# Kernel tuning notes

Hardware: AMD Instinct MI355X
Metric: run time of the kernel (lower is better)

Reference implementation:

```python
import jax, jax.numpy as jnp
import numpy as np

B, S, D = 1, 2048, 4096
H, KV, HD = 32, 8, 128
C = 4096  # cache length
THETA = 1000000.0
NEG = -1e9


def setup_inputs() -> dict:
    key = jax.random.key(0)
    ks = jax.random.split(key, 8)
    std = 0.02
    x = jax.random.normal(ks[0], (B, S, D), jnp.float32)
    wq = jax.random.normal(ks[1], (H * HD, D), jnp.float32) * std
    wk = jax.random.normal(ks[2], (KV * HD, D), jnp.float32) * std
    wv = jax.random.normal(ks[3], (KV * HD, D), jnp.float32) * std
    wo = jax.random.normal(ks[4], (D, H * HD), jnp.float32) * std
    k_cache = jnp.zeros((B, KV, C, HD), jnp.float32)
    v_cache = jnp.zeros((B, KV, C, HD), jnp.float32)
    # rotary tables (real/imag of freqs_cis)
    inv_freq = 1.0 / (THETA ** (jnp.arange(0, HD, 2, dtype=jnp.float32) / HD))  # [HD/2]
    t = jnp.arange(C, dtype=jnp.float32)
    freqs = jnp.outer(t, inv_freq)  # [C, HD/2]
    cos, sin = jnp.cos(freqs), jnp.sin(freqs)
    # causal additive mask over cache positions
    mask = jnp.where(jnp.tril(jnp.ones((C, C), bool)), 0.0, NEG).astype(jnp.float32)
    storage_idx = jnp.arange(S, dtype=jnp.int32)
    return {"x": x, "wq": wq, "wk": wk, "wv": wv, "wo": wo,
            "k_cache": k_cache, "v_cache": v_cache,
            "cos": cos, "sin": sin, "mask": mask, "storage_idx": storage_idx}


def _rope(x, cos, sin):
    # x: [B, h, S, HD]; cos/sin: [S, HD/2] -> complex mult on interleaved pairs
    xr, xi = x[..., 0::2], x[..., 1::2]
    c = cos[None, None, :, :]
    s = sin[None, None, :, :]
    or_, oi_ = xr * c - xi * s, xr * s + xi * c
    return jnp.stack([or_, oi_], axis=-1).reshape(x.shape)


def reference(x, wq, wk, wv, wo, k_cache, v_cache, cos, sin, mask, storage_idx):
    bsz, seqlen, _ = x.shape
    xq = jnp.einsum('bsd,ed->bse', x, wq).reshape(bsz, seqlen, H, HD).transpose(0, 2, 1, 3)
    xk = jnp.einsum('bsd,ed->bse', x, wk).reshape(bsz, seqlen, KV, HD).transpose(0, 2, 1, 3)
    xv = jnp.einsum('bsd,ed->bse', x, wv).reshape(bsz, seqlen, KV, HD).transpose(0, 2, 1, 3)
    cos_g, sin_g = cos[storage_idx], sin[storage_idx]
    xq = _rope(xq, cos_g, sin_g)
    xk = _rope(xk, cos_g, sin_g)
    # scatter into KV cache at storage_idx along the position axis
    keys = k_cache.at[:, :, storage_idx, :].set(xk)
    values = v_cache.at[:, :, storage_idx, :].set(xv)
    # GQA: repeat kv heads (kv-head-major, matches expand+reshape)
    rep = H // KV
    keys = jnp.repeat(keys, rep, axis=1)      # [B, H, C, HD]
    values = jnp.repeat(values, rep, axis=1)  # [B, H, C, HD]
    scores = jnp.einsum('bhqd,bhkd->bhqk', xq, keys) / np.sqrt(HD)
    scores = scores + mask[storage_idx][None, None, :, :]
    attn = jax.nn.softmax(scores, axis=-1)
    out = jnp.einsum('bhqk,bhkd->bhqd', attn, values)
    out = out.transpose(0, 2, 1, 3).reshape(bsz, seqlen, H * HD)
    return jnp.einsum('bse,de->bsd', out, wo)
```

## Files before the change

kernel.cpp:

```cpp
#include <hip/hip_runtime.h>
#include <cstdint>
#include <cstddef>

#define S_LEN 2048
#define DM    4096
#define NH    32
#define NKV   8
#define HDIM  128
#define EQ    4096
#define EKV   1024
#define SCALE 0.08838834764831845f
#define SC_LOG2E 0.1275325477889277f

typedef unsigned short u16;
typedef short bf16x8 __attribute__((ext_vector_type(8)));
typedef float f32x4  __attribute__((ext_vector_type(4)));

__device__ __forceinline__ u16 f2bf(float f) {
  union { float f; unsigned u; } v; v.f = f;
  unsigned r = v.u + 0x7FFFu + ((v.u >> 16) & 1u);
  return (u16)(r >> 16);
}
__device__ __forceinline__ float bf2f(u16 b) {
  union { unsigned u; float f; } v; v.u = ((unsigned)b) << 16;
  return v.f;
}
__device__ __forceinline__ void glds16(const void* g, void* l) {
  __builtin_amdgcn_global_load_lds((const __attribute__((address_space(1))) void*)g,
                                   (__attribute__((address_space(3))) void*)l, 16, 0, 0);
}

__global__ void cast_all(const float* __restrict__ x, const float* __restrict__ wq,
                         const float* __restrict__ wk, const float* __restrict__ wv,
                         const float* __restrict__ wo,
                         u16* __restrict__ xb, u16* __restrict__ wqb,
                         u16* __restrict__ wkb, u16* __restrict__ wvb,
                         u16* __restrict__ wob) {
  const size_t stride = (size_t)gridDim.x * blockDim.x;
  for (size_t u = (size_t)blockIdx.x * blockDim.x + threadIdx.x; u < 12582912u; u += stride) {
    const float* in; u16* outp; size_t i;
    if (u < 2097152u)      { in = x;  outp = xb;  i = u; }
    else if (u < 6291456u) { in = wq; outp = wqb; i = u - 2097152u; }
    else if (u < 7340032u) { in = wk; outp = wkb; i = u - 6291456u; }
    else if (u < 8388608u) { in = wv; outp = wvb; i = u - 7340032u; }
    else                   { in = wo; outp = wob; i = u - 8388608u; }
    float4 f = ((const float4*)in)[i];
    ushort4 b;
    b.x = f2bf(f.x); b.y = f2bf(f.y); b.z = f2bf(f.z); b.w = f2bf(f.w);
    ((ushort4*)outp)[i] = b;
  }
}

template<int UN>
__device__ __forceinline__ void stage_t(const u16* __restrict__ g, int ldg, int k0,
                                        u16* ldsp, int t) {
  const int wb = t & ~63;
#pragma unroll
  for (int j = 0; j < UN / 256; ++j) {
    const int U = j * 256 + t;
    const int row = U >> 3, u = U & 7;
    const int uu = u ^ (row & 7);
    glds16(g + (size_t)row * ldg + k0 + uu * 8, ldsp + (size_t)(j * 256 + wb) * 8);
  }
}

template<int NF, bool QKV3>
__global__ __launch_bounds__(256, 2)
void gemm2p(const u16* __restrict__ A, const u16* __restrict__ B,
            void* __restrict__ Cq, u16* __restrict__ Ck, u16* __restrict__ Cv,
            int K) {
  constexpr int BN = 64 * NF;
  constexpr int AT = 128 * 64;
  constexpr int BT = BN * 64;
  __shared__ u16 lds[2 * (AT + BT)];
  const int t = threadIdx.x;
  const int l = t & 63, lr = l & 15, lg = l >> 4;
  const int wid = t >> 6, wm = wid >> 1, wn = wid & 1;
  const int m0 = blockIdx.y * 128, n0 = blockIdx.x * BN;
  const int KT = K >> 6;

  int axo[2];
  axo[0] = (lg ^ (lr & 7)) * 8;
  axo[1] = ((4 + lg) ^ (lr & 7)) * 8;

  const u16* Ab = A + (size_t)m0 * K;
  const u16* Bb = B + (size_t)n0 * K;

  f32x4 acc[4][2 * NF] = {};

  stage_t<1024>(Ab, K, 0, &lds[0], t);
  stage_t<BT / 8>(Bb, K, 0, &lds[2 * AT], t);
  __syncthreads();

  int cur = 0;
#pragma unroll 1
  for (int tau = 0; tau < KT; ++tau) {
    const int kn = (tau + 1 < KT ? tau + 1 : KT - 1) * 64;
    stage_t<1024>(Ab, K, kn, &lds[(cur ^ 1) * AT], t);
    stage_t<BT / 8>(Bb, K, kn, &lds[2 * AT + (cur ^ 1) * BT], t);

    const int aBase = cur * AT;
    const int bBase = 2 * AT + cur * BT;

    bf16x8 af[4][2];
#pragma unroll
    for (int mf = 0; mf < 4; ++mf)
#pragma unroll
      for (int kk = 0; kk < 2; ++kk) {
        const int row = wm * 64 + mf * 16 + lr;
        af[mf][kk] = *(const bf16x8*)&lds[aBase + row * 64 + axo[kk] + ((row & 7) ? 0 : 0)];
      }
#pragma unroll
    for (int mf = 0; mf < 4; ++mf)
#pragma unroll
      for (int kk = 0; kk < 2; ++kk) {
        const int row = wm * 64 + mf * 16 + lr;
        const int uu = ((kk * 4 + lg) ^ (row & 7)) * 8;
        af[mf][kk] = *(const bf16x8*)&lds[aBase + row * 64 + uu];
      }

#pragma unroll
    for (int n = 0; n < 2 * NF; ++n) {
      const int brow = wn * (32 * NF) + n * 16 + lr;
      const int u0 = ((0 * 4 + lg) ^ (brow & 7)) * 8;
      const int u1 = ((1 * 4 + lg) ^ (brow & 7)) * 8;
      bf16x8 b0 = *(const bf16x8*)&lds[bBase + brow * 64 + u0];
      bf16x8 b1 = *(const bf16x8*)&lds[bBase + brow * 64 + u1];
#pragma unroll
      for (int mf = 0; mf < 4; ++mf) {
        acc[mf][n] = __builtin_amdgcn_mfma_f32_16x16x32_bf16(af[mf][0], b0, acc[mf][n], 0, 0, 0);
        acc[mf][n] = __builtin_amdgcn_mfma_f32_16x16x32_bf16(af[mf][1], b1, acc[mf][n], 0, 0, 0);
      }
    }
    __syncthreads();
    cur ^= 1;
  }

#pragma unroll
  for (int mf = 0; mf < 4; ++mf) {
    const int row = m0 + wm * 64 + mf * 16 + lg * 4;
#pragma unroll
    for (int n = 0; n < 2 * NF; ++n) {
      const int gc = n0 + wn * (32 * NF) + n * 16 + lr;
#pragma unroll
      for (int r = 0; r < 4; ++r) {
        if constexpr (QKV3) {
          if (gc < 4096)
            ((u16*)Cq)[(size_t)(row + r) * 4096 + gc] = f2bf(acc[mf][n][r]);
          else if (gc < 5120)
            Ck[(size_t)(row + r) * 1024 + (gc - 4096)] = f2bf(acc[mf][n][r]);
          else
            Cv[(size_t)(row + r) * 1024 + (gc - 5120)] = f2bf(acc[mf][n][r]);
        } else {
          ((float*)Cq)[(size_t)(row + r) * 4096 + gc] = acc[mf][n][r];
        }
      }
    }
  }
}

__global__ void rope_all(u16* __restrict__ qd, u16* __restrict__ kd,
                         const float* __restrict__ cosb, const float* __restrict__ sinb,
                         const int* __restrict__ sidx) {
  const int u = blockIdx.x * blockDim.x + threadIdx.x;
  u16* base; int s, b;
  if (u < 1048576) {
    base = qd + (size_t)u * 8;
    s = u >> 9;
    b = u & 15;
  } else if (u < 1310720) {
    const int u2 = u - 1048576;
    base = kd + (size_t)u2 * 8;
    s = u2 >> 7;
    b = u2 & 15;
  } else return;
  const int pos = sidx[s];
  const float4 c  = *(const float4*)&cosb[pos * 64 + b * 4];
  const float4 sn = *(const float4*)&sinb[pos * 64 + b * 4];
  uint4 raw = *(uint4*)base;
  u16* pe = (u16*)&raw;
  const float cc[4] = {c.x, c.y, c.z, c.w};
  const float ss[4] = {sn.x, sn.y, sn.z, sn.w};
#pragma unroll
  for (int j = 0; j < 4; ++j) {
    const float xr = bf2f(pe[2 * j]), xi = bf2f(pe[2 * j + 1]);
    pe[2 * j]     = f2bf(xr * cc[j] - xi * ss[j]);
    pe[2 * j + 1] = f2bf(xr * ss[j] + xi * cc[j]);
  }
  *(uint4*)base = raw;
}

__global__ void transpose_v(const u16* __restrict__ v, u16* __restrict__ vt) {
  __shared__ u16 tile[32][33];
  const int tx = threadIdx.x, ty = threadIdx.y;
  const int c0 = blockIdx.x * 32, s0 = blockIdx.y * 32;
#pragma unroll
  for (int j = 0; j < 32; j += 8)
    tile[ty + j][tx] = v[(size_t)(s0 + ty + j) * EKV + c0 + tx];
  __syncthreads();
#pragma unroll
  for (int j = 0; j < 32; j += 8)
    vt[(size_t)(c0 + ty + j) * S_LEN + s0 + tx] = tile[tx][ty + j];
}

__global__ __launch_bounds__(256, 2)
void attn_fwd(const u16* __restrict__ q, const u16* __restrict__ k,
              const u16* __restrict__ vt, u16* __restrict__ ao) {
  __shared__ u16 lK[64 * 128];
  __shared__ u16 lV[128 * 64];
  __shared__ u16 lP[4 * 16 * 72];
  const int t = threadIdx.x, w = t >> 6, l = t & 63;
  const int lr = l & 15, lg = l >> 4;
  const int wb = t & ~63;
  const int p = blockIdx.x, h = blockIdx.y;
  const int kvh = h >> 2;
  u16* lPw = &lP[w * (16 * 72)];

#pragma unroll 1
  for (int ph = 0; ph < 2; ++ph) {
    const int qt = ph ? (31 - p) : p;
    const int q0 = qt * 64 + w * 16;
    const int nt = qt + 1;

    bf16x8 qa[4];
#pragma unroll
    for (int kc = 0; kc < 4; ++kc)
      qa[kc] = *(const bf16x8*)&q[(size_t)(q0 + lr) * EQ + h * HDIM + kc * 32 + lg * 8];

    f32x4 o[8] = {};
    float mrun[4], lrun[4];
#pragma unroll
    for (int r = 0; r < 4; ++r) { mrun[r] = -1e30f; lrun[r] = 0.f; }

    for (int tk = 0; tk < nt; ++tk) {
      const int kv0 = tk * 64;
      __syncthreads();
#pragma unroll
      for (int hh = 0; hh < 4; ++hh) {
        const int f = hh * 256 + t;
        { const int row = f >> 4, u = f & 15, us = u ^ (row & 7);
          glds16(&k[(size_t)(kv0 + row) * EKV + kvh * HDIM + us * 8], &lK[(hh * 256 + wb) * 8]); }
        { const int row = f >> 3, u = f & 7, us = u ^ (row & 7);
          glds16(&vt[(size_t)(kvh * HDIM + row) * S_LEN + kv0 + us * 8], &lV[(hh * 256 + wb) * 8]); }
      }
      __syncthreads();

      f32x4 sc[4] = {};
#pragma unroll
      for (int n = 0; n < 4; ++n) {
#pragma unroll
        for (int kc = 0; kc < 4; ++kc) {
          const int row = n * 16 + lr;
          const int us = (kc * 4 + lg) ^ (row & 7);
          bf16x8 bk = *(const bf16x8*)&lK[row * 128 + us * 8];
          sc[n] = __builtin_amdgcn_mfma_f32_16x16x32_bf16(qa[kc], bk, sc[n], 0, 0, 0);
        }
      }

#pragma unroll
      for (int n = 0; n < 4; ++n) {
        const int kvc = kv0 + n * 16 + lr;
#pragma unroll
        for (int r = 0; r < 4; ++r) {
          const int qr = q0 + lg * 4 + r;
          const float v = sc[n][r] * SC_LOG2E;
          sc[n][r] = (kvc > qr) ? -1e30f : v;
        }
      }
#pragma unroll
      for (int r = 0; r < 4; ++r) {
        float v = fmaxf(fmaxf(sc[0][r], sc[1][r]), fmaxf(sc[2][r], sc[3][r]));
        v = fmaxf(v, __shfl_xor(v, 1));
        v = fmaxf(v, __shfl_xor(v, 2));
        v = fmaxf(v, __shfl_xor(v, 4));
        v = fmaxf(v, __shfl_xor(v, 8));
        const float mn = fmaxf(mrun[r], v);
        const float sf = __builtin_amdgcn_exp2f(mrun[r] - mn);
        mrun[r] = mn;
        float rs = 0.f;
#pragma unroll
        for (int n = 0; n < 4; ++n) {
          const float pv = __builtin_amdgcn_exp2f(sc[n][r] - mn);
          sc[n][r] = pv;
          rs += pv;
        }
        rs += __shfl_xor(rs, 1);
        rs += __shfl_xor(rs, 2);
        rs += __shfl_xor(rs, 4);
        rs += __shfl_xor(rs, 8);
        lrun[r] = lrun[r] * sf + rs;
#pragma unroll
        for (int nh = 0; nh < 8; ++nh) o[nh][r] *= sf;
      }
#pragma unroll
      for (int n = 0; n < 4; ++n)
#pragma unroll
        for (int r = 0; r < 4; ++r)
          lPw[(lg * 4 + r) * 72 + n * 16 + lr] = f2bf(sc[n][r]);

#pragma unroll
      for (int kc2 = 0; kc2 < 2; ++kc2) {
        bf16x8 pa = *(const bf16x8*)&lPw[lr * 72 + kc2 * 32 + lg * 8];
#pragma unroll
        for (int nh = 0; nh < 8; ++nh) {
          const int row = nh * 16 + lr;
          const int us = (kc2 * 4 + lg) ^ (row & 7);
          bf16x8 bv = *(const bf16x8*)&lV[row * 64 + us * 8];
          o[nh] = __builtin_amdgcn_mfma_f32_16x16x32_bf16(pa, bv, o[nh], 0, 0, 0);
        }
      }
    }

#pragma unroll
    for (int nh = 0; nh < 8; ++nh)
#pragma unroll
      for (int r = 0; r < 4; ++r) {
        const float val = o[nh][r] / lrun[r];
        ao[(size_t)(q0 + lg * 4 + r) * EQ + h * HDIM + nh * 16 + lr] = f2bf(val);
      }
  }
}

extern "C" void kernel_launch(void* const* d_in, const int* in_sizes, int n_in,
                              void* d_out, int out_size, void* d_ws, size_t ws_size,
                              hipStream_t stream) {
  (void)in_sizes; (void)n_in; (void)out_size; (void)ws_size;
  const float* x    = (const float*)d_in[0];
  const float* wq   = (const float*)d_in[1];
  const float* wk   = (const float*)d_in[2];
  const float* wv   = (const float*)d_in[3];
  const float* wo   = (const float*)d_in[4];
  const float* cosb = (const float*)d_in[7];
  const float* sinb = (const float*)d_in[8];
  const int*   sidx = (const int*)d_in[10];
  float* out = (float*)d_out;

  u16* ws  = (u16*)d_ws;
  u16* xb  = ws;
  u16* wqb = xb  + (size_t)S_LEN * DM;
  u16* wkb = wqb + (size_t)EQ * DM;
  u16* wvb = wkb + (size_t)EKV * DM;
  u16* wob = wvb + (size_t)EKV * DM;
  u16* qb  = wob + (size_t)DM * EQ;
  u16* kb  = qb  + (size_t)S_LEN * EQ;
  u16* vb  = kb  + (size_t)S_LEN * EKV;
  u16* vtb = vb  + (size_t)S_LEN * EKV;
  u16* aob = vtb + (size_t)S_LEN * EKV;

  cast_all<<<2048, 256, 0, stream>>>(x, wq, wk, wv, wo, xb, wqb, wkb, wvb, wob);
  gemm2p<3, true><<<dim3(32, 16), 256, 0, stream>>>(xb, wqb, qb, kb, vb, DM);
  rope_all<<<5120, 256, 0, stream>>>(qb, kb, cosb, sinb, sidx);
  transpose_v<<<dim3(EKV / 32, S_LEN / 32), dim3(32, 8), 0, stream>>>(vb, vtb);
  attn_fwd<<<dim3(16, NH), 256, 0, stream>>>(qb, kb, vtb, aob);
  gemm2p<2, false><<<dim3(32, 16), 256, 0, stream>>>(aob, wob, out, nullptr, nullptr, EQ);
}
```

Baseline: 322.7 us.

## Restructure GEMMs to two-wave 128-thread blocks and double-buffer attention K/V tiles

The GEMM kernel now runs with 128 threads (two waves), each wave owning a full 128-row strip and a narrower column slice. The tile shapes stay the same, but each wave holds more accumulators and gets more register-level reuse of the A fragments. The attention kernel double-buffers the K and V tiles in LDS, prefetching the next tile while the current one is computed, which removes one barrier per iteration. The trade-offs are fewer waves per CU in the GEMMs, which may hurt latency hiding, and double the LDS footprint in attention, which could limit occupancy.

```diff
diff --git a/kernel.cpp b/kernel.cpp
--- a/kernel.cpp
+++ b/kernel.cpp
@@ -9,7 +9,6 @@
 #define HDIM  128
 #define EQ    4096
 #define EKV   1024
-#define SCALE 0.08838834764831845f
 #define SC_LOG2E 0.1275325477889277f
 
 typedef unsigned short u16;
@@ -52,107 +51,94 @@
 }
 
 template<int UN>
-__device__ __forceinline__ void stage_t(const u16* __restrict__ g, int ldg, int k0,
-                                        u16* ldsp, int t) {
+__device__ __forceinline__ void stage128(const u16* __restrict__ g, int ldg, int k0,
+                                         u16* ldsp, int t) {
   const int wb = t & ~63;
 #pragma unroll
-  for (int j = 0; j < UN / 256; ++j) {
-    const int U = j * 256 + t;
+  for (int j = 0; j < UN / 128; ++j) {
+    const int U = j * 128 + t;
     const int row = U >> 3, u = U & 7;
     const int uu = u ^ (row & 7);
-    glds16(g + (size_t)row * ldg + k0 + uu * 8, ldsp + (size_t)(j * 256 + wb) * 8);
-  }
-}
-
-template<int NF, bool QKV3>
-__global__ __launch_bounds__(256, 2)
-void gemm2p(const u16* __restrict__ A, const u16* __restrict__ B,
+    glds16(g + (size_t)row * ldg + k0 + uu * 8, ldsp + (size_t)(j * 128 + wb) * 8);
+  }
+}
+
+template<int FN, bool QKV3>
+__global__ __launch_bounds__(128, 1)
+void gemm2w(const u16* __restrict__ A, const u16* __restrict__ B,
             void* __restrict__ Cq, u16* __restrict__ Ck, u16* __restrict__ Cv,
             int K) {
-  constexpr int BN = 64 * NF;
+  constexpr int BN = 32 * FN;
   constexpr int AT = 128 * 64;
   constexpr int BT = BN * 64;
   __shared__ u16 lds[2 * (AT + BT)];
   const int t = threadIdx.x;
   const int l = t & 63, lr = l & 15, lg = l >> 4;
-  const int wid = t >> 6, wm = wid >> 1, wn = wid & 1;
+  const int wn = t >> 6;
   const int m0 = blockIdx.y * 128, n0 = blockIdx.x * BN;
   const int KT = K >> 6;
 
-  int axo[2];
-  axo[0] = (lg ^ (lr & 7)) * 8;
-  axo[1] = ((4 + lg) ^ (lr & 7)) * 8;
-
   const u16* Ab = A + (size_t)m0 * K;
   const u16* Bb = B + (size_t)n0 * K;
 
-  f32x4 acc[4][2 * NF] = {};
-
-  stage_t<1024>(Ab, K, 0, &lds[0], t);
-  stage_t<BT / 8>(Bb, K, 0, &lds[2 * AT], t);
+  f32x4 acc[8][FN] = {};
+
+  stage128<1024>(Ab, K, 0, &lds[0], t);
+  stage128<BT / 8>(Bb, K, 0, &lds[2 * AT], t);
   __syncthreads();
 
   int cur = 0;
 #pragma unroll 1
   for (int tau = 0; tau < KT; ++tau) {
     const int kn = (tau + 1 < KT ? tau + 1 : KT - 1) * 64;
-    stage_t<1024>(Ab, K, kn, &lds[(cur ^ 1) * AT], t);
-    stage_t<BT / 8>(Bb, K, kn, &lds[2 * AT + (cur ^ 1) * BT], t);
-
-    const int aBase = cur * AT;
-    const int bBase = 2 * AT + cur * BT;
-
-    bf16x8 af[4][2];
-#pragma unroll
-    for (int mf = 0; mf < 4; ++mf)
-#pragma unroll
-      for (int kk = 0; kk < 2; ++kk) {
-        const int row = wm * 64 + mf * 16 + lr;
-        af[mf][kk] = *(const bf16x8*)&lds[aBase + row * 64 + axo[kk] + ((row & 7) ? 0 : 0)];
-      }
-#pragma unroll
-    for (int mf = 0; mf < 4; ++mf)
-#pragma unroll
-      for (int kk = 0; kk < 2; ++kk) {
-        const int row = wm * 64 + mf * 16 + lr;
-        const int uu = ((kk * 4 + lg) ^ (row & 7)) * 8;
-        af[mf][kk] = *(const bf16x8*)&lds[aBase + row * 64 + uu];
-      }
-
-#pragma unroll
-    for (int n = 0; n < 2 * NF; ++n) {
-      const int brow = wn * (32 * NF) + n * 16 + lr;
-      const int u0 = ((0 * 4 + lg) ^ (brow & 7)) * 8;
-      const int u1 = ((1 * 4 + lg) ^ (brow & 7)) * 8;
-      bf16x8 b0 = *(const bf16x8*)&lds[bBase + brow * 64 + u0];
-      bf16x8 b1 = *(const bf16x8*)&lds[bBase + brow * 64 + u1];
-#pragma unroll
-      for (int mf = 0; mf < 4; ++mf) {
-        acc[mf][n] = __builtin_amdgcn_mfma_f32_16x16x32_bf16(af[mf][0], b0, acc[mf][n], 0, 0, 0);
-        acc[mf][n] = __builtin_amdgcn_mfma_f32_16x16x32_bf16(af[mf][1], b1, acc[mf][n], 0, 0, 0);
-      }
+    stage128<1024>(Ab, K, kn, &lds[(cur ^ 1) * AT], t);
+    stage128<BT / 8>(Bb, K, kn, &lds[2 * AT + (cur ^ 1) * BT], t);
+
+    const int aB = cur * AT;
+    const int bB = 2 * AT + cur * BT;
+
+#pragma unroll
+    for (int kk = 0; kk < 2; ++kk) {
+      bf16x8 af[8], bf[FN];
+#pragma unroll
+      for (int mf = 0; mf < 8; ++mf) {
+        const int row = mf * 16 + lr;
+        const int us = ((kk * 4 + lg) ^ (row & 7)) * 8;
+        af[mf] = *(const bf16x8*)&lds[aB + row * 64 + us];
+      }
+#pragma unroll
+      for (int nf = 0; nf < FN; ++nf) {
+        const int row = wn * (16 * FN) + nf * 16 + lr;
+        const int us = ((kk * 4 + lg) ^ (row & 7)) * 8;
+        bf[nf] = *(const bf16x8*)&lds[bB + row * 64 + us];
+      }
+#pragma unroll
+      for (int mf = 0; mf < 8; ++mf)
+#pragma unroll
+        for (int nf = 0; nf < FN; ++nf)
+          acc[mf][nf] = __builtin_amdgcn_mfma_f32_16x16x32_bf16(af[mf], bf[nf], acc[mf][nf], 0, 0, 0);
     }
     __syncthreads();
     cur ^= 1;
   }
 
 #pragma unroll
-  for (int mf = 0; mf < 4; ++mf) {
-    const int row = m0 + wm * 64 + mf * 16 + lg * 4;
-#pragma unroll
-    for (int n = 0; n < 2 * NF; ++n) {
-      const int gc = n0 + wn * (32 * NF) + n * 16 + lr;
+  for (int mf = 0; mf < 8; ++mf) {
+    const int row = m0 + mf * 16 + lg * 4;
+#pragma unroll
+    for (int nf = 0; nf < FN; ++nf) {
+      const int gc = n0 + wn * (16 * FN) + nf * 16 + lr;
 #pragma unroll
       for (int r = 0; r < 4; ++r) {
         if constexpr (QKV3) {
           if (gc < 4096)
-            ((u16*)Cq)[(size_t)(row + r) * 4096 + gc] = f2bf(acc[mf][n][r]);
+            ((u16*)Cq)[(size_t)(row + r) * 4096 + gc] = f2bf(acc[mf][nf][r]);
           else if (gc < 5120)
-            Ck[(size_t)(row + r) * 1024 + (gc - 4096)] = f2bf(acc[mf][n][r]);
+            Ck[(size_t)(row + r) * 1024 + (gc - 4096)] = f2bf(acc[mf][nf][r]);
           else
-            Cv[(size_t)(row + r) * 1024 + (gc - 5120)] = f2bf(acc[mf][n][r]);
+            Cv[(size_t)(row + r) * 1024 + (gc - 5120)] = f2bf(acc[mf][nf][r]);
         } else {
-          ((float*)Cq)[(size_t)(row + r) * 4096 + gc] = acc[mf][n][r];
+          ((float*)Cq)[(size_t)(row + r) * 4096 + gc] = acc[mf][nf][r];
         }
       }
     }
@@ -203,11 +189,22 @@
     vt[(size_t)(c0 + ty + j) * S_LEN + s0 + tx] = tile[tx][ty + j];
 }
 
+#define ATTN_STAGE(TK, BUF) { \
+  const int kv0s = (TK) * 64; \
+  _Pragma("unroll") \
+  for (int hh = 0; hh < 4; ++hh) { \
+    const int f = hh * 256 + t; \
+    { const int row = f >> 4, uu = f & 15, us = uu ^ (row & 7); \
+      glds16(&k[(size_t)(kv0s + row) * EKV + kvh * HDIM + us * 8], &lK[BUF][(hh * 256 + wb) * 8]); } \
+    { const int row = f >> 3, uu = f & 7, us = uu ^ (row & 7); \
+      glds16(&vt[(size_t)(kvh * HDIM + row) * S_LEN + kv0s + us * 8], &lV[BUF][(hh * 256 + wb) * 8]); } \
+  } }
+
 __global__ __launch_bounds__(256, 2)
 void attn_fwd(const u16* __restrict__ q, const u16* __restrict__ k,
               const u16* __restrict__ vt, u16* __restrict__ ao) {
-  __shared__ u16 lK[64 * 128];
-  __shared__ u16 lV[128 * 64];
+  __shared__ u16 lK[2][64 * 128];
+  __shared__ u16 lV[2][128 * 64];
   __shared__ u16 lP[4 * 16 * 72];
   const int t = threadIdx.x, w = t >> 6, l = t & 63;
   const int lr = l & 15, lg = l >> 4;
@@ -232,18 +229,16 @@
 #pragma unroll
     for (int r = 0; r < 4; ++r) { mrun[r] = -1e30f; lrun[r] = 0.f; }
 
+    int cur = 0;
+    ATTN_STAGE(0, 0);
+    __syncthreads();
+
+#pragma unroll 1
     for (int tk = 0; tk < nt; ++tk) {
       const int kv0 = tk * 64;
-      __syncthreads();
-#pragma unroll
-      for (int hh = 0; hh < 4; ++hh) {
-        const int f = hh * 256 + t;
-        { const int row = f >> 4, u = f & 15, us = u ^ (row & 7);
-          glds16(&k[(size_t)(kv0 + row) * EKV + kvh * HDIM + us * 8], &lK[(hh * 256 + wb) * 8]); }
-        { const int row = f >> 3, u = f & 7, us = u ^ (row & 7);
-          glds16(&vt[(size_t)(kvh * HDIM + row) * S_LEN + kv0 + us * 8], &lV[(hh * 256 + wb) * 8]); }
-      }
-      __syncthreads();
+      if (tk + 1 < nt) ATTN_STAGE(tk + 1, cur ^ 1);
+      const u16* lKc = lK[cur];
+      const u16* lVc = lV[cur];
 
       f32x4 sc[4] = {};
 #pragma unroll
@@ -252,7 +247,7 @@
         for (int kc = 0; kc < 4; ++kc) {
           const int row = n * 16 + lr;
           const int us = (kc * 4 + lg) ^ (row & 7);
-          bf16x8 bk = *(const bf16x8*)&lK[row * 128 + us * 8];
+          bf16x8 bk = *(const bf16x8*)&lKc[row * 128 + us * 8];
           sc[n] = __builtin_amdgcn_mfma_f32_16x16x32_bf16(qa[kc], bk, sc[n], 0, 0, 0);
         }
       }
@@ -305,10 +300,12 @@
         for (int nh = 0; nh < 8; ++nh) {
           const int row = nh * 16 + lr;
           const int us = (kc2 * 4 + lg) ^ (row & 7);
-          bf16x8 bv = *(const bf16x8*)&lV[row * 64 + us * 8];
+          bf16x8 bv = *(const bf16x8*)&lVc[row * 64 + us * 8];
           o[nh] = __builtin_amdgcn_mfma_f32_16x16x32_bf16(pa, bv, o[nh], 0, 0, 0);
         }
       }
+      __syncthreads();
+      cur ^= 1;
     }
 
 #pragma unroll
@@ -348,9 +345,9 @@
   u16* aob = vtb + (size_t)S_LEN * EKV;
 
   cast_all<<<2048, 256, 0, stream>>>(x, wq, wk, wv, wo, xb, wqb, wkb, wvb, wob);
-  gemm2p<3, true><<<dim3(32, 16), 256, 0, stream>>>(xb, wqb, qb, kb, vb, DM);
+  gemm2w<6, true><<<dim3(32, 16), 128, 0, stream>>>(xb, wqb, qb, kb, vb, DM);
   rope_all<<<5120, 256, 0, stream>>>(qb, kb, cosb, sinb, sidx);
   transpose_v<<<dim3(EKV / 32, S_LEN / 32), dim3(32, 8), 0, stream>>>(vb, vtb);
   attn_fwd<<<dim3(16, NH), 256, 0, stream>>>(qb, kb, vtb, aob);
-  gemm2p<2, false><<<dim3(32, 16), 256, 0, stream>>>(aob, wob, out, nullptr, nullptr, EQ);
-}
+  gemm2w<4, false><<<dim3(32, 16), 128, 0, stream>>>(aob, wob, out, nullptr, nullptr, EQ);
+}
```

Result: slower. 370.7 us (+14.9%).

## Fuse paired query tiles over shared KV loads with double-buffered LDS staging

Applied to the files above, without the earlier changes.

The attention kernel now processes both of its paired query tiles (p and 31-p) in a single pass over KV tiles instead of two separate phases. Each K/V tile is loaded into LDS once and used by both query tiles, which removes the duplicate loads of the shared prefix. Loads for the next tile are issued into a second LDS buffer while the current one is computed, overlapping memory with MFMA work. The cost is double the LDS for K/V and two sets of accumulators and Q fragments per wave, so register pressure goes up and occupancy may drop. A redundant duplicated A-fragment LDS load in the GEMM is also removed.

```diff
diff --git a/kernel.cpp b/kernel.cpp
--- a/kernel.cpp
+++ b/kernel.cpp
@@ -9,7 +9,6 @@
 #define HDIM  128
 #define EQ    4096
 #define EKV   1024
-#define SCALE 0.08838834764831845f
 #define SC_LOG2E 0.1275325477889277f
 
 typedef unsigned short u16;
@@ -79,10 +78,6 @@
   const int m0 = blockIdx.y * 128, n0 = blockIdx.x * BN;
   const int KT = K >> 6;
 
-  int axo[2];
-  axo[0] = (lg ^ (lr & 7)) * 8;
-  axo[1] = ((4 + lg) ^ (lr & 7)) * 8;
-
   const u16* Ab = A + (size_t)m0 * K;
   const u16* Bb = B + (size_t)n0 * K;
 
@@ -103,13 +98,6 @@
     const int bBase = 2 * AT + cur * BT;
 
     bf16x8 af[4][2];
-#pragma unroll
-    for (int mf = 0; mf < 4; ++mf)
-#pragma unroll
-      for (int kk = 0; kk < 2; ++kk) {
-        const int row = wm * 64 + mf * 16 + lr;
-        af[mf][kk] = *(const bf16x8*)&lds[aBase + row * 64 + axo[kk] + ((row & 7) ? 0 : 0)];
-      }
 #pragma unroll
     for (int mf = 0; mf < 4; ++mf)
 #pragma unroll
@@ -203,11 +191,86 @@
     vt[(size_t)(c0 + ty + j) * S_LEN + s0 + tx] = tile[tx][ty + j];
 }
 
+#define ATTN_STAGE(TK, BUF) { \
+  const int kv0s = (TK) * 64; \
+  _Pragma("unroll") \
+  for (int hh = 0; hh < 4; ++hh) { \
+    const int f = hh * 256 + t; \
+    { const int row = f >> 4, uu = f & 15, us = uu ^ (row & 7); \
+      glds16(&k[(size_t)(kv0s + row) * EKV + kvh * HDIM + us * 8], &lK[BUF][(hh * 256 + wb) * 8]); } \
+    { const int row = f >> 3, uu = f & 7, us = uu ^ (row & 7); \
+      glds16(&vt[(size_t)(kvh * HDIM + row) * S_LEN + kv0s + us * 8], &lV[BUF][(hh * 256 + wb) * 8]); } \
+  } }
+
+#define TILE_STEP(QA, O, MR, LR, Q0) { \
+  f32x4 sc[4] = {}; \
+  _Pragma("unroll") \
+  for (int n = 0; n < 4; ++n) { \
+    _Pragma("unroll") \
+    for (int kc = 0; kc < 4; ++kc) { \
+      const int row = n * 16 + lr; \
+      const int us = (kc * 4 + lg) ^ (row & 7); \
+      bf16x8 bk = *(const bf16x8*)&lKc[row * 128 + us * 8]; \
+      sc[n] = __builtin_amdgcn_mfma_f32_16x16x32_bf16(QA[kc], bk, sc[n], 0, 0, 0); \
+    } \
+  } \
+  _Pragma("unroll") \
+  for (int n = 0; n < 4; ++n) { \
+    const int kvc = kv0 + n * 16 + lr; \
+    _Pragma("unroll") \
+    for (int r = 0; r < 4; ++r) { \
+      const int qr = (Q0) + lg * 4 + r; \
+      const float vv = sc[n][r] * SC_LOG2E; \
+      sc[n][r] = (kvc > qr) ? -1e30f : vv; \
+    } \
+  } \
+  _Pragma("unroll") \
+  for (int r = 0; r < 4; ++r) { \
+    float v = fmaxf(fmaxf(sc[0][r], sc[1][r]), fmaxf(sc[2][r], sc[3][r])); \
+    v = fmaxf(v, __shfl_xor(v, 1)); \
+    v = fmaxf(v, __shfl_xor(v, 2)); \
+    v = fmaxf(v, __shfl_xor(v, 4)); \
+    v = fmaxf(v, __shfl_xor(v, 8)); \
+    const float mn = fmaxf(MR[r], v); \
+    const float sf = __builtin_amdgcn_exp2f(MR[r] - mn); \
+    MR[r] = mn; \
+    float rs = 0.f; \
+    _Pragma("unroll") \
+    for (int n = 0; n < 4; ++n) { \
+      const float pv = __builtin_amdgcn_exp2f(sc[n][r] - mn); \
+      sc[n][r] = pv; \
+      rs += pv; \
+    } \
+    rs += __shfl_xor(rs, 1); \
+    rs += __shfl_xor(rs, 2); \
+    rs += __shfl_xor(rs, 4); \
+    rs += __shfl_xor(rs, 8); \
+    LR[r] = LR[r] * sf + rs; \
+    _Pragma("unroll") \
+    for (int nh = 0; nh < 8; ++nh) O[nh][r] *= sf; \
+  } \
+  _Pragma("unroll") \
+  for (int n = 0; n < 4; ++n) \
+    _Pragma("unroll") \
+    for (int r = 0; r < 4; ++r) \
+      lPw[(lg * 4 + r) * 72 + n * 16 + lr] = f2bf(sc[n][r]); \
+  _Pragma("unroll") \
+  for (int kc2 = 0; kc2 < 2; ++kc2) { \
+    bf16x8 pa = *(const bf16x8*)&lPw[lr * 72 + kc2 * 32 + lg * 8]; \
+    _Pragma("unroll") \
+    for (int nh = 0; nh < 8; ++nh) { \
+      const int row = nh * 16 + lr; \
+      const int us = (kc2 * 4 + lg) ^ (row & 7); \
+      bf16x8 bv = *(const bf16x8*)&lVc[row * 64 + us * 8]; \
+      O[nh] = __builtin_amdgcn_mfma_f32_16x16x32_bf16(pa, bv, O[nh], 0, 0, 0); \
+    } \
+  } }
+
 __global__ __launch_bounds__(256, 2)
 void attn_fwd(const u16* __restrict__ q, const u16* __restrict__ k,
               const u16* __restrict__ vt, u16* __restrict__ ao) {
-  __shared__ u16 lK[64 * 128];
-  __shared__ u16 lV[128 * 64];
+  __shared__ u16 lK[2][64 * 128];
+  __shared__ u16 lV[2][128 * 64];
   __shared__ u16 lP[4 * 16 * 72];
   const int t = threadIdx.x, w = t >> 6, l = t & 63;
   const int lr = l & 15, lg = l >> 4;
@@ -216,109 +279,49 @@
   const int kvh = h >> 2;
   u16* lPw = &lP[w * (16 * 72)];
 
+  const int q0A = p * 64 + w * 16;
+  const int q0B = (31 - p) * 64 + w * 16;
+  const int nt = 32 - p;
+
+  bf16x8 qaA[4], qaB[4];
+#pragma unroll
+  for (int kc = 0; kc < 4; ++kc) {
+    qaA[kc] = *(const bf16x8*)&q[(size_t)(q0A + lr) * EQ + h * HDIM + kc * 32 + lg * 8];
+    qaB[kc] = *(const bf16x8*)&q[(size_t)(q0B + lr) * EQ + h * HDIM + kc * 32 + lg * 8];
+  }
+
+  f32x4 oA[8] = {}, oB[8] = {};
+  float mA[4], lA[4], mB[4], lB[4];
+#pragma unroll
+  for (int r = 0; r < 4; ++r) { mA[r] = -1e30f; lA[r] = 0.f; mB[r] = -1e30f; lB[r] = 0.f; }
+
+  int cur = 0;
+  ATTN_STAGE(0, 0);
+  __syncthreads();
+
 #pragma unroll 1
-  for (int ph = 0; ph < 2; ++ph) {
-    const int qt = ph ? (31 - p) : p;
-    const int q0 = qt * 64 + w * 16;
-    const int nt = qt + 1;
-
-    bf16x8 qa[4];
-#pragma unroll
-    for (int kc = 0; kc < 4; ++kc)
-      qa[kc] = *(const bf16x8*)&q[(size_t)(q0 + lr) * EQ + h * HDIM + kc * 32 + lg * 8];
-
-    f32x4 o[8] = {};
-    float mrun[4], lrun[4];
-#pragma unroll
-    for (int r = 0; r < 4; ++r) { mrun[r] = -1e30f; lrun[r] = 0.f; }
-
-    for (int tk = 0; tk < nt; ++tk) {
-      const int kv0 = tk * 64;
-      __syncthreads();
-#pragma unroll
-      for (int hh = 0; hh < 4; ++hh) {
-        const int f = hh * 256 + t;
-        { const int row = f >> 4, u = f & 15, us = u ^ (row & 7);
-          glds16(&k[(size_t)(kv0 + row) * EKV + kvh * HDIM + us * 8], &lK[(hh * 256 + wb) * 8]); }
-        { const int row = f >> 3, u = f & 7, us = u ^ (row & 7);
-          glds16(&vt[(size_t)(kvh * HDIM + row) * S_LEN + kv0 + us * 8], &lV[(hh * 256 + wb) * 8]); }
-      }
-      __syncthreads();
-
-      f32x4 sc[4] = {};
-#pragma unroll
-      for (int n = 0; n < 4; ++n) {
-#pragma unroll
-        for (int kc = 0; kc < 4; ++kc) {
-          const int row = n * 16 + lr;
-          const int us = (kc * 4 + lg) ^ (row & 7);
-          bf16x8 bk = *(const bf16x8*)&lK[row * 128 + us * 8];
-          sc[n] = __builtin_amdgcn_mfma_f32_16x16x32_bf16(qa[kc], bk, sc[n], 0, 0, 0);
-        }
-      }
-
-#pragma unroll
-      for (int n = 0; n < 4; ++n) {
-        const int kvc = kv0 + n * 16 + lr;
-#pragma unroll
-        for (int r = 0; r < 4; ++r) {
-          const int qr = q0 + lg * 4 + r;
-          const float v = sc[n][r] * SC_LOG2E;
-          sc[n][r] = (kvc > qr) ? -1e30f : v;
-        }
-      }
-#pragma unroll
-      for (int r = 0; r < 4; ++r) {
-        float v = fmaxf(fmaxf(sc[0][r], sc[1][r]), fmaxf(sc[2][r], sc[3][r]));
-        v = fmaxf(v, __shfl_xor(v, 1));
-        v = fmaxf(v, __shfl_xor(v, 2));
-        v = fmaxf(v, __shfl_xor(v, 4));
-        v = fmaxf(v, __shfl_xor(v, 8));
-        const float mn = fmaxf(mrun[r], v);
-        const float sf = __builtin_amdgcn_exp2f(mrun[r] - mn);
-        mrun[r] = mn;
-        float rs = 0.f;
-#pragma unroll
-        for (int n = 0; n < 4; ++n) {
-          const float pv = __builtin_amdgcn_exp2f(sc[n][r] - mn);
-          sc[n][r] = pv;
-          rs += pv;
-        }
-        rs += __shfl_xor(rs, 1);
-        rs += __shfl_xor(rs, 2);
-        rs += __shfl_xor(rs, 4);
-        rs += __shfl_xor(rs, 8);
-        lrun[r] = lrun[r] * sf + rs;
-#pragma unroll
-        for (int nh = 0; nh < 8; ++nh) o[nh][r] *= sf;
-      }
-#pragma unroll
-      for (int n = 0; n < 4; ++n)
-#pragma unroll
-        for (int r = 0; r < 4; ++r)
-          lPw[(lg * 4 + r) * 72 + n * 16 + lr] = f2bf(sc[n][r]);
-
-#pragma unroll
-      for (int kc2 = 0; kc2 < 2; ++kc2) {
-        bf16x8 pa = *(const bf16x8*)&lPw[lr * 72 + kc2 * 32 + lg * 8];
-#pragma unroll
-        for (int nh = 0; nh < 8; ++nh) {
-          const int row = nh * 16 + lr;
-          const int us = (kc2 * 4 + lg) ^ (row & 7);
-          bf16x8 bv = *(const bf16x8*)&lV[row * 64 + us * 8];
-          o[nh] = __builtin_amdgcn_mfma_f32_16x16x32_bf16(pa, bv, o[nh], 0, 0, 0);
-        }
-      }
+  for (int tk = 0; tk < nt; ++tk) {
+    const int kv0 = tk * 64;
+    if (tk + 1 < nt) ATTN_STAGE(tk + 1, cur ^ 1);
+    const u16* lKc = lK[cur];
+    const u16* lVc = lV[cur];
+
+    TILE_STEP(qaB, oB, mB, lB, q0B);
+    if (tk <= p) {
+      TILE_STEP(qaA, oA, mA, lA, q0A);
     }
-
-#pragma unroll
-    for (int nh = 0; nh < 8; ++nh)
-#pragma unroll
-      for (int r = 0; r < 4; ++r) {
-        const float val = o[nh][r] / lrun[r];
-        ao[(size_t)(q0 + lg * 4 + r) * EQ + h * HDIM + nh * 16 + lr] = f2bf(val);
-      }
-  }
+    __syncthreads();
+    cur ^= 1;
+  }
+
+#pragma unroll
+  for (int nh = 0; nh < 8; ++nh)
+#pragma unroll
+    for (int r = 0; r < 4; ++r) {
+      const int col = h * HDIM + nh * 16 + lr;
+      ao[(size_t)(q0A + lg * 4 + r) * EQ + col] = f2bf(oA[nh][r] / lA[r]);
+      ao[(size_t)(q0B + lg * 4 + r) * EQ + col] = f2bf(oB[nh][r] / lB[r]);
+    }
 }
 
 extern "C" void kernel_launch(void* const* d_in, const int* in_sizes, int n_in,
```

Result: no change. 320.7 us (-0.6%).

## Double-buffer K/V tiles in attention and remap GEMM blocks per XCD

Applied to the files above, without the earlier changes.

The attention kernel now keeps two LDS buffers for K and V, so the next KV tile is prefetched while the current tile is computed. This removes one barrier per iteration and hides global-to-LDS load latency, at the cost of doubled K/V LDS use, which may limit occupancy. Both GEMM launches switch to a 1D grid with a block-ID remap that gives each XCD a contiguous group of N tiles, aimed at better L2 reuse. A redundant A-fragment LDS load that was immediately overwritten is also removed.

```diff
diff --git a/kernel.cpp b/kernel.cpp
--- a/kernel.cpp
+++ b/kernel.cpp
@@ -9,7 +9,6 @@
 #define HDIM  128
 #define EQ    4096
 #define EKV   1024
-#define SCALE 0.08838834764831845f
 #define SC_LOG2E 0.1275325477889277f
 
 typedef unsigned short u16;
@@ -76,12 +75,13 @@
   const int t = threadIdx.x;
   const int l = t & 63, lr = l & 15, lg = l >> 4;
   const int wid = t >> 6, wm = wid >> 1, wn = wid & 1;
-  const int m0 = blockIdx.y * 128, n0 = blockIdx.x * BN;
+
+  const int bid = blockIdx.x;
+  const int xcd = bid & 7, j = bid >> 3;
+  const int bx = xcd * 4 + (j >> 4);
+  const int by = j & 15;
+  const int m0 = by * 128, n0 = bx * BN;
   const int KT = K >> 6;
-
-  int axo[2];
-  axo[0] = (lg ^ (lr & 7)) * 8;
-  axo[1] = ((4 + lg) ^ (lr & 7)) * 8;
 
   const u16* Ab = A + (size_t)m0 * K;
   const u16* Bb = B + (size_t)n0 * K;
@@ -103,13 +103,6 @@
     const int bBase = 2 * AT + cur * BT;
 
     bf16x8 af[4][2];
-#pragma unroll
-    for (int mf = 0; mf < 4; ++mf)
-#pragma unroll
-      for (int kk = 0; kk < 2; ++kk) {
-        const int row = wm * 64 + mf * 16 + lr;
-        af[mf][kk] = *(const bf16x8*)&lds[aBase + row * 64 + axo[kk] + ((row & 7) ? 0 : 0)];
-      }
 #pragma unroll
     for (int mf = 0; mf < 4; ++mf)
 #pragma unroll
@@ -203,11 +196,22 @@
     vt[(size_t)(c0 + ty + j) * S_LEN + s0 + tx] = tile[tx][ty + j];
 }
 
+#define ATTN_STAGE(TK, BUF) { \
+  const int kv0s = (TK) * 64; \
+  _Pragma("unroll") \
+  for (int hh = 0; hh < 4; ++hh) { \
+    const int f = hh * 256 + t; \
+    { const int row = f >> 4, uu = f & 15, us = uu ^ (row & 7); \
+      glds16(&k[(size_t)(kv0s + row) * EKV + kvh * HDIM + us * 8], &lK[BUF][(hh * 256 + wb) * 8]); } \
+    { const int row = f >> 3, uu = f & 7, us = uu ^ (row & 7); \
+      glds16(&vt[(size_t)(kvh * HDIM + row) * S_LEN + kv0s + us * 8], &lV[BUF][(hh * 256 + wb) * 8]); } \
+  } }
+
 __global__ __launch_bounds__(256, 2)
 void attn_fwd(const u16* __restrict__ q, const u16* __restrict__ k,
               const u16* __restrict__ vt, u16* __restrict__ ao) {
-  __shared__ u16 lK[64 * 128];
-  __shared__ u16 lV[128 * 64];
+  __shared__ u16 lK[2][64 * 128];
+  __shared__ u16 lV[2][128 * 64];
   __shared__ u16 lP[4 * 16 * 72];
   const int t = threadIdx.x, w = t >> 6, l = t & 63;
   const int lr = l & 15, lg = l >> 4;
@@ -232,18 +236,16 @@
 #pragma unroll
     for (int r = 0; r < 4; ++r) { mrun[r] = -1e30f; lrun[r] = 0.f; }
 
+    int cur = 0;
+    ATTN_STAGE(0, 0);
+    __syncthreads();
+
+#pragma unroll 1
     for (int tk = 0; tk < nt; ++tk) {
       const int kv0 = tk * 64;
-      __syncthreads();
-#pragma unroll
-      for (int hh = 0; hh < 4; ++hh) {
-        const int f = hh * 256 + t;
-        { const int row = f >> 4, u = f & 15, us = u ^ (row & 7);
-          glds16(&k[(size_t)(kv0 + row) * EKV + kvh * HDIM + us * 8], &lK[(hh * 256 + wb) * 8]); }
-        { const int row = f >> 3, u = f & 7, us = u ^ (row & 7);
-          glds16(&vt[(size_t)(kvh * HDIM + row) * S_LEN + kv0 + us * 8], &lV[(hh * 256 + wb) * 8]); }
-      }
-      __syncthreads();
+      if (tk + 1 < nt) ATTN_STAGE(tk + 1, cur ^ 1);
+      const u16* lKc = lK[cur];
+      const u16* lVc = lV[cur];
 
       f32x4 sc[4] = {};
 #pragma unroll
@@ -252,7 +254,7 @@
         for (int kc = 0; kc < 4; ++kc) {
           const int row = n * 16 + lr;
           const int us = (kc * 4 + lg) ^ (row & 7);
-          bf16x8 bk = *(const bf16x8*)&lK[row * 128 + us * 8];
+          bf16x8 bk = *(const bf16x8*)&lKc[row * 128 + us * 8];
           sc[n] = __builtin_amdgcn_mfma_f32_16x16x32_bf16(qa[kc], bk, sc[n], 0, 0, 0);
         }
       }
@@ -305,10 +307,12 @@
         for (int nh = 0; nh < 8; ++nh) {
           const int row = nh * 16 + lr;
           const int us = (kc2 * 4 + lg) ^ (row & 7);
-          bf16x8 bv = *(const bf16x8*)&lV[row * 64 + us * 8];
+          bf16x8 bv = *(const bf16x8*)&lVc[row * 64 + us * 8];
           o[nh] = __builtin_amdgcn_mfma_f32_16x16x32_bf16(pa, bv, o[nh], 0, 0, 0);
         }
       }
+      __syncthreads();
+      cur ^= 1;
     }
 
 #pragma unroll
@@ -348,9 +352,9 @@
   u16* aob = vtb + (size_t)S_LEN * EKV;
 
   cast_all<<<2048, 256, 0, stream>>>(x, wq, wk, wv, wo, xb, wqb, wkb, wvb, wob);
-  gemm2p<3, true><<<dim3(32, 16), 256, 0, stream>>>(xb, wqb, qb, kb, vb, DM);
+  gemm2p<3, true><<<512, 256, 0, stream>>>(xb, wqb, qb, kb, vb, DM);
   rope_all<<<5120, 256, 0, stream>>>(qb, kb, cosb, sinb, sidx);
   transpose_v<<<dim3(EKV / 32, S_LEN / 32), dim3(32, 8), 0, stream>>>(vb, vtb);
   attn_fwd<<<dim3(16, NH), 256, 0, stream>>>(qb, kb, vtb, aob);
-  gemm2p<2, false><<<dim3(32, 16), 256, 0, stream>>>(aob, wob, out, nullptr, nullptr, EQ);
-}
+  gemm2p<2, false><<<512, 256, 0, stream>>>(aob, wob, out, nullptr, nullptr, EQ);
+}
```

New measurement: 321.6 us. About the same (-0.3%).
